# Optimization experiments

Measured on AMD Instinct MI355X. Metric: run time of the kernel, lower is better.

## Reference

```python
import jax, jax.numpy as jnp
import numpy as np

EPS = 1e-6

def setup_inputs() -> dict:
    key = jax.random.key(0)
    k1, k2, k3 = jax.random.split(key, 3)
    N, L, S, H, D = 4, 4096, 4096, 8, 64
    queries = jax.random.normal(k1, (N, L, H, D), dtype=jnp.float32)
    keys = jax.random.normal(k2, (N, S, H, D), dtype=jnp.float32)
    values = jax.random.normal(k3, (N, S, H, D), dtype=jnp.float32)
    return {"queries": queries, "keys": keys, "values": values}

def _feature_map(x):
    # elu(x) + 1
    return jax.nn.elu(x) + 1.0

def reference(queries, keys, values):
    Q = _feature_map(queries)          # [N, L, H, D]
    K = _feature_map(keys)             # [N, S, H, D]
    v_length = values.shape[1]
    v = values / v_length              # [N, S, H, Dv]
    # KV outer-product sum over source positions: [N, H, D, Dv]
    KV = jnp.einsum('nshd,nshv->nhdv', K, v)
    # Normalizer: Q . sum_s K  -> [N, L, H]
    Z = 1.0 / (jnp.einsum('nlhd,nhd->nlh', Q, K.sum(axis=1)) + EPS)
    # Queried values: [N, L, H, Dv]
    out = jnp.einsum('nlhd,nhdv,nlh->nlhv', Q, KV, Z) * v_length
    return out
```

## Files before the change

kernel.cpp:

```cpp
#include <hip/hip_runtime.h>

#define NB   4
#define LQ   4096
#define SK   4096
#define NHD  8
#define DD   64
#define ROWSTRIDE (NHD * DD)
#define CH   16
#define SROWS (SK / CH)
#define TS   16
#define KVSZ (DD * DD)
#define PART_STRIDE (KVSZ + DD)
#define NHTOT (NB * NHD)
#define LT   64
#define EPSF 1e-6f

__device__ __forceinline__ float fmap(float x) {
    return x > 0.f ? x + 1.f : __expf(x);
}

__global__ __launch_bounds__(256) void k1_kv(const float* __restrict__ Kin,
                                             const float* __restrict__ Vin,
                                             float* __restrict__ part) {
    const int blk   = blockIdx.x;
    const int nh    = blk / CH;
    const int chunk = blk % CH;
    const int n = nh / NHD, h = nh % NHD;
    const int t = threadIdx.x;
    const int r  = t >> 4;
    const int c  = (t & 15) << 2;
    const int d0 = c;
    const int e0 = r << 2;

    __shared__ __align__(16) float Ks[TS][DD];
    __shared__ __align__(16) float Vs[TS][DD];
    __shared__ __align__(16) float ksred[TS][DD];

    float acc[4][4] = {};
    float ksl[4] = {0.f, 0.f, 0.f, 0.f};

    const size_t base = ((size_t)n * SK + (size_t)chunk * SROWS) * ROWSTRIDE
                        + (size_t)h * DD;

    for (int s0 = 0; s0 < SROWS; s0 += TS) {
        const size_t g = base + (size_t)(s0 + r) * ROWSTRIDE + c;
        float4 kg = *(const float4*)(Kin + g);
        float4 vg = *(const float4*)(Vin + g);
        float4 kf;
        kf.x = fmap(kg.x); kf.y = fmap(kg.y); kf.z = fmap(kg.z); kf.w = fmap(kg.w);
        ksl[0] += kf.x; ksl[1] += kf.y; ksl[2] += kf.z; ksl[3] += kf.w;
        __syncthreads();
        *(float4*)&Ks[r][c] = kf;
        *(float4*)&Vs[r][c] = vg;
        __syncthreads();
#pragma unroll
        for (int s = 0; s < TS; ++s) {
            float4 k4 = *(float4*)&Ks[s][d0];
            float4 v4 = *(float4*)&Vs[s][e0];
            float kk[4] = {k4.x, k4.y, k4.z, k4.w};
            float vv[4] = {v4.x, v4.y, v4.z, v4.w};
#pragma unroll
            for (int i = 0; i < 4; ++i)
#pragma unroll
                for (int j = 0; j < 4; ++j)
                    acc[i][j] += kk[i] * vv[j];
        }
    }

    __syncthreads();
    *(float4*)&ksred[r][c] = make_float4(ksl[0], ksl[1], ksl[2], ksl[3]);
    __syncthreads();

    float* pb = part + ((size_t)nh * CH + chunk) * PART_STRIDE;
    if (t < DD) {
        float s = 0.f;
#pragma unroll
        for (int rr = 0; rr < TS; ++rr) s += ksred[rr][t];
        pb[KVSZ + t] = s;
    }
#pragma unroll
    for (int i = 0; i < 4; ++i) {
        float4 o = make_float4(acc[i][0], acc[i][1], acc[i][2], acc[i][3]);
        *(float4*)(pb + (d0 + i) * DD + e0) = o;
    }
}

__global__ __launch_bounds__(256) void k2_reduce(const float* __restrict__ part,
                                                 float* __restrict__ fin) {
    const int idx = blockIdx.x * 256 + threadIdx.x;
    if (idx >= NHTOT * PART_STRIDE) return;
    const int nh = idx / PART_STRIDE;
    const int j  = idx - nh * PART_STRIDE;
    const float* p = part + (size_t)nh * CH * PART_STRIDE + j;
    float s = 0.f;
#pragma unroll
    for (int cix = 0; cix < CH; ++cix) s += p[(size_t)cix * PART_STRIDE];
    fin[idx] = s;
}

#define QPAD 68
__global__ __launch_bounds__(256) void k3_out(const float* __restrict__ Qin,
                                              const float* __restrict__ fin,
                                              float* __restrict__ out) {
    const int blk = blockIdx.x;
    const int nh  = blk >> 6;
    const int lc  = blk & 63;
    const int n = nh >> 3, h = nh & 7;
    const int t = threadIdx.x;

    __shared__ __align__(16) float KVs[DD][DD];
    __shared__ __align__(16) float Ksm[DD];
    __shared__ __align__(16) float Qs[LT][QPAD];

    const float* fb = fin + (size_t)nh * PART_STRIDE;
    float* kvflat = &KVs[0][0];
    for (int i = t * 4; i < KVSZ; i += 1024)
        *(float4*)(kvflat + i) = *(const float4*)(fb + i);
    if (t < DD) Ksm[t] = fb[KVSZ + t];

    const int r = t >> 4;
    const int c = (t & 15) << 2;
    const size_t qbase = ((size_t)n * LQ + (size_t)lc * LT) * ROWSTRIDE
                         + (size_t)h * DD;
    for (int rr = r; rr < LT; rr += 16) {
        float4 q = *(const float4*)(Qin + qbase + (size_t)rr * ROWSTRIDE + c);
        float4 qf;
        qf.x = fmap(q.x); qf.y = fmap(q.y); qf.z = fmap(q.z); qf.w = fmap(q.w);
        *(float4*)&Qs[rr][c] = qf;
    }
    __syncthreads();

    const int e0 = (t & 15) << 2;
    const int l0 = (t >> 4) << 2;
    float acc[4][4] = {};
    float z[4] = {0.f, 0.f, 0.f, 0.f};

#pragma unroll 4
    for (int d0 = 0; d0 < DD; d0 += 4) {
        float4 km4 = *(float4*)&Ksm[d0];
        float km[4] = {km4.x, km4.y, km4.z, km4.w};
        float q[4][4];
        float kv[4][4];
#pragma unroll
        for (int i = 0; i < 4; ++i) {
            float4 q4 = *(float4*)&Qs[l0 + i][d0];
            q[i][0] = q4.x; q[i][1] = q4.y; q[i][2] = q4.z; q[i][3] = q4.w;
        }
#pragma unroll
        for (int s = 0; s < 4; ++s) {
            float4 kv4 = *(float4*)&KVs[d0 + s][e0];
            kv[s][0] = kv4.x; kv[s][1] = kv4.y; kv[s][2] = kv4.z; kv[s][3] = kv4.w;
        }
#pragma unroll
        for (int i = 0; i < 4; ++i)
#pragma unroll
            for (int s = 0; s < 4; ++s) {
                z[i] += q[i][s] * km[s];
#pragma unroll
                for (int j = 0; j < 4; ++j)
                    acc[i][j] += q[i][s] * kv[s][j];
            }
    }

#pragma unroll
    for (int i = 0; i < 4; ++i) {
        float zi = 1.f / (z[i] + EPSF);
        float4 o = make_float4(acc[i][0] * zi, acc[i][1] * zi,
                               acc[i][2] * zi, acc[i][3] * zi);
        *(float4*)(out + ((size_t)n * LQ + (size_t)lc * LT + l0 + i) * ROWSTRIDE
                   + (size_t)h * DD + e0) = o;
    }
}

extern "C" void kernel_launch(void* const* d_in, const int* in_sizes, int n_in,
                              void* d_out, int out_size, void* d_ws, size_t ws_size,
                              hipStream_t stream) {
    const float* Q = (const float*)d_in[0];
    const float* K = (const float*)d_in[1];
    const float* V = (const float*)d_in[2];
    float* out = (float*)d_out;

    float* ws   = (float*)d_ws;
    float* part = ws;
    float* fin  = ws + (size_t)NHTOT * CH * PART_STRIDE;

    k1_kv<<<NHTOT * CH, 256, 0, stream>>>(K, V, part);
    k2_reduce<<<(NHTOT * PART_STRIDE + 255) / 256, 256, 0, stream>>>(part, fin);
    k3_out<<<NHTOT * (LQ / LT), 256, 0, stream>>>(Q, fin, out);
}
```

Measured before the change: 162.4 us.

## Retile KV and output kernels with 8x8 register tiles, prefetch, bf16 Q staging

```diff
diff --git a/kernel.cpp b/kernel.cpp
--- a/kernel.cpp
+++ b/kernel.cpp
@@ -5,83 +5,169 @@
 #define SK   4096
 #define NHD  8
 #define DD   64
-#define ROWSTRIDE (NHD * DD)
-#define CH   16
-#define SROWS (SK / CH)
-#define TS   16
-#define KVSZ (DD * DD)
+#define ROWSTRIDE 512
+#define NHTOT 32
+#define EPSF 1e-6f
+
+#define CH     32
+#define SROWS  (SK / CH)
+#define TS     32
+#define NITER  (SROWS / TS)
+#define KVSZ   (DD * DD)
 #define PART_STRIDE (KVSZ + DD)
-#define NHTOT (NB * NHD)
-#define LT   64
-#define EPSF 1e-6f
+
+#define KS_OFF   0
+#define VS_OFF   2048
+#define KRED_OFF 4096
+#define BUF_PAD  66
+#define BUFA_OFF 0
+#define BUFB_OFF 4224
+#define SM_FLOATS 8448
 
 __device__ __forceinline__ float fmap(float x) {
     return x > 0.f ? x + 1.f : __expf(x);
 }
-
-__global__ __launch_bounds__(256) void k1_kv(const float* __restrict__ Kin,
-                                             const float* __restrict__ Vin,
-                                             float* __restrict__ part) {
+__device__ __forceinline__ float4 fmap4(float4 v) {
+    return make_float4(fmap(v.x), fmap(v.y), fmap(v.z), fmap(v.w));
+}
+__device__ __forceinline__ unsigned short f2bf(float f) {
+    unsigned int u = __float_as_uint(f);
+    return (unsigned short)((u + 0x7fffu + ((u >> 16) & 1u)) >> 16);
+}
+
+__global__ __launch_bounds__(256, 4) void k1_kv(const float* __restrict__ Kin,
+                                                const float* __restrict__ Vin,
+                                                float* __restrict__ part) {
+    __shared__ float sm[SM_FLOATS];
     const int blk   = blockIdx.x;
-    const int nh    = blk / CH;
-    const int chunk = blk % CH;
-    const int n = nh / NHD, h = nh % NHD;
+    const int nh    = blk >> 5;
+    const int chunk = blk & 31;
+    const int n = nh >> 3, h = nh & 7;
     const int t = threadIdx.x;
-    const int r  = t >> 4;
-    const int c  = (t & 15) << 2;
-    const int d0 = c;
-    const int e0 = r << 2;
-
-    __shared__ __align__(16) float Ks[TS][DD];
-    __shared__ __align__(16) float Vs[TS][DD];
-    __shared__ __align__(16) float ksred[TS][DD];
-
-    float acc[4][4] = {};
+    const int w = t >> 6, lane = t & 63;
+    const int d0 = (lane & 7) * 8;
+    const int e0 = (lane >> 3) * 8;
+    const int r = t >> 4;
+    const int c = (t & 15) * 4;
+
+    const size_t gbase = ((size_t)n * SK + (size_t)chunk * SROWS) * ROWSTRIDE
+                         + (size_t)h * DD + c;
+    const float* Kb = Kin + gbase;
+    const float* Vb = Vin + gbase;
+
+    float acc[8][8] = {};
     float ksl[4] = {0.f, 0.f, 0.f, 0.f};
 
-    const size_t base = ((size_t)n * SK + (size_t)chunk * SROWS) * ROWSTRIDE
-                        + (size_t)h * DD;
-
-    for (int s0 = 0; s0 < SROWS; s0 += TS) {
-        const size_t g = base + (size_t)(s0 + r) * ROWSTRIDE + c;
-        float4 kg = *(const float4*)(Kin + g);
-        float4 vg = *(const float4*)(Vin + g);
-        float4 kf;
-        kf.x = fmap(kg.x); kf.y = fmap(kg.y); kf.z = fmap(kg.z); kf.w = fmap(kg.w);
-        ksl[0] += kf.x; ksl[1] += kf.y; ksl[2] += kf.z; ksl[3] += kf.w;
+    float4 ka = *(const float4*)(Kb + (size_t)r * ROWSTRIDE);
+    float4 kb = *(const float4*)(Kb + (size_t)(r + 16) * ROWSTRIDE);
+    float4 va = *(const float4*)(Vb + (size_t)r * ROWSTRIDE);
+    float4 vb = *(const float4*)(Vb + (size_t)(r + 16) * ROWSTRIDE);
+
+    for (int it = 0; it < NITER; ++it) {
+        float4 kfa = fmap4(ka), kfb = fmap4(kb);
+        ksl[0] += kfa.x + kfb.x; ksl[1] += kfa.y + kfb.y;
+        ksl[2] += kfa.z + kfb.z; ksl[3] += kfa.w + kfb.w;
         __syncthreads();
-        *(float4*)&Ks[r][c] = kf;
-        *(float4*)&Vs[r][c] = vg;
+        *(float4*)&sm[KS_OFF + r * DD + c]        = kfa;
+        *(float4*)&sm[KS_OFF + (r + 16) * DD + c] = kfb;
+        *(float4*)&sm[VS_OFF + r * DD + c]        = va;
+        *(float4*)&sm[VS_OFF + (r + 16) * DD + c] = vb;
         __syncthreads();
-#pragma unroll
-        for (int s = 0; s < TS; ++s) {
-            float4 k4 = *(float4*)&Ks[s][d0];
-            float4 v4 = *(float4*)&Vs[s][e0];
-            float kk[4] = {k4.x, k4.y, k4.z, k4.w};
-            float vv[4] = {v4.x, v4.y, v4.z, v4.w};
-#pragma unroll
-            for (int i = 0; i < 4; ++i)
-#pragma unroll
-                for (int j = 0; j < 4; ++j)
+        if (it + 1 < NITER) {
+            const size_t o = (size_t)(it + 1) * TS * ROWSTRIDE;
+            ka = *(const float4*)(Kb + o + (size_t)r * ROWSTRIDE);
+            kb = *(const float4*)(Kb + o + (size_t)(r + 16) * ROWSTRIDE);
+            va = *(const float4*)(Vb + o + (size_t)r * ROWSTRIDE);
+            vb = *(const float4*)(Vb + o + (size_t)(r + 16) * ROWSTRIDE);
+        }
+        const int sbase = w * 8;
+#pragma unroll
+        for (int s = 0; s < 8; ++s) {
+            const float* kr = &sm[KS_OFF + (sbase + s) * DD + d0];
+            const float* vr = &sm[VS_OFF + (sbase + s) * DD + e0];
+            float4 kA = *(const float4*)kr,       kB = *(const float4*)(kr + 4);
+            float4 vA = *(const float4*)vr,       vB = *(const float4*)(vr + 4);
+            float kk[8] = {kA.x, kA.y, kA.z, kA.w, kB.x, kB.y, kB.z, kB.w};
+            float vv[8] = {vA.x, vA.y, vA.z, vA.w, vB.x, vB.y, vB.z, vB.w};
+#pragma unroll
+            for (int i = 0; i < 8; ++i)
+#pragma unroll
+                for (int j = 0; j < 8; ++j)
                     acc[i][j] += kk[i] * vv[j];
         }
     }
 
-    __syncthreads();
-    *(float4*)&ksred[r][c] = make_float4(ksl[0], ksl[1], ksl[2], ksl[3]);
-    __syncthreads();
-
-    float* pb = part + ((size_t)nh * CH + chunk) * PART_STRIDE;
-    if (t < DD) {
-        float s = 0.f;
-#pragma unroll
-        for (int rr = 0; rr < TS; ++rr) s += ksred[rr][t];
-        pb[KVSZ + t] = s;
-    }
-#pragma unroll
-    for (int i = 0; i < 4; ++i) {
-        float4 o = make_float4(acc[i][0], acc[i][1], acc[i][2], acc[i][3]);
-        *(float4*)(pb + (d0 + i) * DD + e0) = o;
+    *(float4*)&sm[KRED_OFF + r * DD + c] = make_float4(ksl[0], ksl[1], ksl[2], ksl[3]);
+    __syncthreads();
+    float ksumF = 0.f;
+    if (w == 0) {
+#pragma unroll
+        for (int rr = 0; rr < 16; ++rr) ksumF += sm[KRED_OFF + rr * DD + lane];
+    }
+    __syncthreads();
+
+    if (w == 2) {
+#pragma unroll
+        for (int i = 0; i < 8; ++i)
+#pragma unroll
+            for (int j = 0; j < 8; j += 2)
+                *(float2*)&sm[BUFA_OFF + (d0 + i) * BUF_PAD + e0 + j] =
+                    make_float2(acc[i][j], acc[i][j + 1]);
+    }
+    if (w == 3) {
+#pragma unroll
+        for (int i = 0; i < 8; ++i)
+#pragma unroll
+            for (int j = 0; j < 8; j += 2)
+                *(float2*)&sm[BUFB_OFF + (d0 + i) * BUF_PAD + e0 + j] =
+                    make_float2(acc[i][j], acc[i][j + 1]);
+    }
+    __syncthreads();
+    if (w == 0) {
+#pragma unroll
+        for (int i = 0; i < 8; ++i)
+#pragma unroll
+            for (int j = 0; j < 8; j += 2) {
+                float2 u = *(float2*)&sm[BUFA_OFF + (d0 + i) * BUF_PAD + e0 + j];
+                acc[i][j] += u.x; acc[i][j + 1] += u.y;
+            }
+    }
+    if (w == 1) {
+#pragma unroll
+        for (int i = 0; i < 8; ++i)
+#pragma unroll
+            for (int j = 0; j < 8; j += 2) {
+                float2 u = *(float2*)&sm[BUFB_OFF + (d0 + i) * BUF_PAD + e0 + j];
+                acc[i][j] += u.x; acc[i][j + 1] += u.y;
+            }
+    }
+    __syncthreads();
+    if (w == 1) {
+#pragma unroll
+        for (int i = 0; i < 8; ++i)
+#pragma unroll
+            for (int j = 0; j < 8; j += 2)
+                *(float2*)&sm[BUFA_OFF + (d0 + i) * BUF_PAD + e0 + j] =
+                    make_float2(acc[i][j], acc[i][j + 1]);
+    }
+    __syncthreads();
+    if (w == 0) {
+#pragma unroll
+        for (int i = 0; i < 8; ++i)
+#pragma unroll
+            for (int j = 0; j < 8; j += 2) {
+                float2 u = *(float2*)&sm[BUFA_OFF + (d0 + i) * BUF_PAD + e0 + j];
+                acc[i][j] += u.x; acc[i][j + 1] += u.y;
+            }
+        float* pb = part + ((size_t)nh * CH + chunk) * PART_STRIDE;
+#pragma unroll
+        for (int i = 0; i < 8; ++i) {
+            *(float4*)(pb + (d0 + i) * DD + e0) =
+                make_float4(acc[i][0], acc[i][1], acc[i][2], acc[i][3]);
+            *(float4*)(pb + (d0 + i) * DD + e0 + 4) =
+                make_float4(acc[i][4], acc[i][5], acc[i][6], acc[i][7]);
+        }
+        pb[KVSZ + lane] = ksumF;
     }
 }
 
@@ -94,81 +180,89 @@
     const float* p = part + (size_t)nh * CH * PART_STRIDE + j;
     float s = 0.f;
 #pragma unroll
-    for (int cix = 0; cix < CH; ++cix) s += p[(size_t)cix * PART_STRIDE];
+    for (int cx = 0; cx < CH; ++cx) s += p[(size_t)cx * PART_STRIDE];
     fin[idx] = s;
 }
 
-#define QPAD 68
-__global__ __launch_bounds__(256) void k3_out(const float* __restrict__ Qin,
-                                              const float* __restrict__ fin,
-                                              float* __restrict__ out) {
+#define LT3  128
+#define QSTR 72
+__global__ __launch_bounds__(128, 2) void k3_out(const float* __restrict__ Qin,
+                                                 const float* __restrict__ fin,
+                                                 float* __restrict__ out) {
+    __shared__ unsigned short Qs[LT3 * QSTR];
+    __shared__ float KVs[DD * DD];
+    __shared__ float Ksm[DD];
     const int blk = blockIdx.x;
-    const int nh  = blk >> 6;
-    const int lc  = blk & 63;
+    const int nh  = blk >> 5;
+    const int lc  = blk & 31;
     const int n = nh >> 3, h = nh & 7;
     const int t = threadIdx.x;
-
-    __shared__ __align__(16) float KVs[DD][DD];
-    __shared__ __align__(16) float Ksm[DD];
-    __shared__ __align__(16) float Qs[LT][QPAD];
+    const int w = t >> 6, lane = t & 63;
 
     const float* fb = fin + (size_t)nh * PART_STRIDE;
-    float* kvflat = &KVs[0][0];
-    for (int i = t * 4; i < KVSZ; i += 1024)
-        *(float4*)(kvflat + i) = *(const float4*)(fb + i);
+    for (int i = t * 4; i < KVSZ; i += 512)
+        *(float4*)&KVs[i] = *(const float4*)(fb + i);
     if (t < DD) Ksm[t] = fb[KVSZ + t];
 
-    const int r = t >> 4;
-    const int c = (t & 15) << 2;
-    const size_t qbase = ((size_t)n * LQ + (size_t)lc * LT) * ROWSTRIDE
-                         + (size_t)h * DD;
-    for (int rr = r; rr < LT; rr += 16) {
-        float4 q = *(const float4*)(Qin + qbase + (size_t)rr * ROWSTRIDE + c);
-        float4 qf;
-        qf.x = fmap(q.x); qf.y = fmap(q.y); qf.z = fmap(q.z); qf.w = fmap(q.w);
-        *(float4*)&Qs[rr][c] = qf;
-    }
-    __syncthreads();
-
-    const int e0 = (t & 15) << 2;
-    const int l0 = (t >> 4) << 2;
-    float acc[4][4] = {};
-    float z[4] = {0.f, 0.f, 0.f, 0.f};
-
-#pragma unroll 4
-    for (int d0 = 0; d0 < DD; d0 += 4) {
-        float4 km4 = *(float4*)&Ksm[d0];
-        float km[4] = {km4.x, km4.y, km4.z, km4.w};
-        float q[4][4];
-        float kv[4][4];
-#pragma unroll
-        for (int i = 0; i < 4; ++i) {
-            float4 q4 = *(float4*)&Qs[l0 + i][d0];
-            q[i][0] = q4.x; q[i][1] = q4.y; q[i][2] = q4.z; q[i][3] = q4.w;
-        }
-#pragma unroll
-        for (int s = 0; s < 4; ++s) {
-            float4 kv4 = *(float4*)&KVs[d0 + s][e0];
-            kv[s][0] = kv4.x; kv[s][1] = kv4.y; kv[s][2] = kv4.z; kv[s][3] = kv4.w;
-        }
-#pragma unroll
-        for (int i = 0; i < 4; ++i)
-#pragma unroll
-            for (int s = 0; s < 4; ++s) {
-                z[i] += q[i][s] * km[s];
-#pragma unroll
-                for (int j = 0; j < 4; ++j)
-                    acc[i][j] += q[i][s] * kv[s][j];
-            }
-    }
-
-#pragma unroll
-    for (int i = 0; i < 4; ++i) {
+    const int r = t >> 4, c = (t & 15) * 4;
+    const float* Qb = Qin + ((size_t)n * LQ + (size_t)lc * LT3) * ROWSTRIDE
+                      + (size_t)h * DD + c;
+    for (int rr = r; rr < LT3; rr += 8) {
+        float4 q = *(const float4*)(Qb + (size_t)rr * ROWSTRIDE);
+        float4 qf = fmap4(q);
+        unsigned int w0 = (unsigned int)f2bf(qf.x) | ((unsigned int)f2bf(qf.y) << 16);
+        unsigned int w1 = (unsigned int)f2bf(qf.z) | ((unsigned int)f2bf(qf.w) << 16);
+        *(uint2*)&Qs[rr * QSTR + c] = make_uint2(w0, w1);
+    }
+    __syncthreads();
+
+    const int e0 = (lane >> 3) * 8;
+    const int rbase = w * 64 + (lane & 7);
+    float acc[8][8] = {};
+    float z[8] = {};
+
+#pragma unroll
+    for (int dch = 0; dch < DD; dch += 4) {
+        float4 km4 = *(const float4*)&Ksm[dch];
+        float kmv[4] = {km4.x, km4.y, km4.z, km4.w};
+        float qf[8][4];
+#pragma unroll
+        for (int i = 0; i < 8; ++i) {
+            uint2 qw = *(const uint2*)&Qs[(rbase + 8 * i) * QSTR + dch];
+            qf[i][0] = __uint_as_float(qw.x << 16);
+            qf[i][1] = __uint_as_float(qw.x & 0xffff0000u);
+            qf[i][2] = __uint_as_float(qw.y << 16);
+            qf[i][3] = __uint_as_float(qw.y & 0xffff0000u);
+        }
+        float kv[4][8];
+#pragma unroll
+        for (int dd = 0; dd < 4; ++dd) {
+            float4 a = *(const float4*)&KVs[(dch + dd) * DD + e0];
+            float4 b = *(const float4*)&KVs[(dch + dd) * DD + e0 + 4];
+            kv[dd][0] = a.x; kv[dd][1] = a.y; kv[dd][2] = a.z; kv[dd][3] = a.w;
+            kv[dd][4] = b.x; kv[dd][5] = b.y; kv[dd][6] = b.z; kv[dd][7] = b.w;
+        }
+#pragma unroll
+        for (int i = 0; i < 8; ++i)
+#pragma unroll
+            for (int dd = 0; dd < 4; ++dd) {
+                z[i] += qf[i][dd] * kmv[dd];
+#pragma unroll
+                for (int j = 0; j < 8; ++j)
+                    acc[i][j] += qf[i][dd] * kv[dd][j];
+            }
+    }
+
+    float* ob = out + ((size_t)n * LQ + (size_t)lc * LT3) * ROWSTRIDE
+                + (size_t)h * DD;
+#pragma unroll
+    for (int i = 0; i < 8; ++i) {
         float zi = 1.f / (z[i] + EPSF);
-        float4 o = make_float4(acc[i][0] * zi, acc[i][1] * zi,
-                               acc[i][2] * zi, acc[i][3] * zi);
-        *(float4*)(out + ((size_t)n * LQ + (size_t)lc * LT + l0 + i) * ROWSTRIDE
-                   + (size_t)h * DD + e0) = o;
+        const size_t row = (size_t)(rbase + 8 * i) * ROWSTRIDE;
+        *(float4*)(ob + row + e0) =
+            make_float4(acc[i][0] * zi, acc[i][1] * zi, acc[i][2] * zi, acc[i][3] * zi);
+        *(float4*)(ob + row + e0 + 4) =
+            make_float4(acc[i][4] * zi, acc[i][5] * zi, acc[i][6] * zi, acc[i][7] * zi);
     }
 }
 
@@ -186,5 +280,5 @@
 
     k1_kv<<<NHTOT * CH, 256, 0, stream>>>(K, V, part);
     k2_reduce<<<(NHTOT * PART_STRIDE + 255) / 256, 256, 0, stream>>>(part, fin);
-    k3_out<<<NHTOT * (LQ / LT), 256, 0, stream>>>(Q, fin, out);
-}
+    k3_out<<<NHTOT * (LQ / LT3), 128, 0, stream>>>(Q, fin, out);
+}
```

Result: slower. 216.1 us (+33.0%).
